# Performance work log

Hardware: AMD Instinct MI355X
Metric: run time of the kernel (lower is better)

## Reference

```python
import jax, jax.numpy as jnp
import numpy as np

B, CIN, H, W = 8, 512, 32, 32
NH = 8
DQ = DK = DV = 256  # int(0.5 * Cin)
COUT = 512


def setup_inputs() -> dict:
    key = jax.random.key(0)
    k0, k1, k2, k3, k4 = jax.random.split(key, 5)
    x = jax.random.normal(k0, (B, CIN, H, W), dtype=jnp.float32)
    # 1x1 conv weights stored as [out, in] matrices (kernel size 1)
    w_qkv = jax.random.normal(k1, (DQ + DK + DV, CIN), dtype=jnp.float32) * 0.02
    b_qkv = jax.random.normal(k2, (DQ + DK + DV,), dtype=jnp.float32) * 0.02
    w_attn = jax.random.normal(k3, (COUT, DV), dtype=jnp.float32) * 0.02
    b_attn = jax.random.normal(k4, (COUT,), dtype=jnp.float32) * 0.02
    return {"x": x, "w_qkv": w_qkv, "b_qkv": b_qkv, "w_attn": w_attn, "b_attn": b_attn}


def _split_heads(t):
    b, c, h, w = t.shape
    return t.reshape(b, NH, c // NH, h, w)


def reference(x, w_qkv, b_qkv, w_attn, b_attn):
    b, _, h, w = x.shape
    hw = h * w
    # 1x1 conv == per-pixel GEMM
    qkv = jnp.einsum('bchw,oc->bohw', x, w_qkv) + b_qkv[None, :, None, None]
    q = qkv[:, :DQ]
    k = qkv[:, DQ:DQ + DK]
    v = qkv[:, DQ + DK:]
    dkh = DK // NH
    q = _split_heads(q) * (dkh ** -0.5)
    k = _split_heads(k)
    v = _split_heads(v)
    flat_q = q.reshape(b, NH, DQ // NH, hw)
    flat_k = k.reshape(b, NH, DK // NH, hw)
    flat_v = v.reshape(b, NH, DV // NH, hw)
    # logits: [b, NH, hw, hw]  (q^T k over feature dim)
    logits = jnp.einsum('bndq,bndk->bnqk', flat_q, flat_k)
    # FAITHFUL quirk: softmax over the HEAD axis (dim=1), as in the source
    weights = jax.nn.softmax(logits, axis=1)
    # attn_out: [b, NH, hw, dvh]
    attn_out = jnp.einsum('bnqk,bndk->bnqd', weights, flat_v)
    # FAITHFUL quirk: raw reshape (no transpose) to [b, NH, dvh, H, W]
    attn_out = attn_out.reshape(b, NH, DV // NH, h, w).reshape(b, DV, h, w)
    out = jnp.einsum('bchw,oc->bohw', attn_out, w_attn) + b_attn[None, :, None, None]
    return out
```

## Files before the change

kernel.cpp:

```cpp
#include <hip/hip_runtime.h>
#include <math.h>

#define BATCH 8
#define CIN   512
#define DQKV  768
#define NHEAD 8
#define HW    1024

typedef __attribute__((ext_vector_type(8))) short  short8;
typedef __attribute__((ext_vector_type(4))) float  float4v;

__device__ __forceinline__ ushort f2bf(float f) {
    union { float f; unsigned u; } c; c.f = f;
    unsigned u = c.u + 0x7fffu + ((c.u >> 16) & 1u);
    return (ushort)(u >> 16);
}

__device__ __forceinline__ void async_ld16(const ushort* g, ushort* l) {
    auto gp = (const __attribute__((address_space(1))) unsigned int*)g;
    auto lp = (__attribute__((address_space(3))) unsigned int*)l;
    __builtin_amdgcn_global_load_lds(gp, lp, 16, 0, 0);
}

__global__ __launch_bounds__(256)
void transpose_cvt(const float* __restrict__ in, ushort* __restrict__ out,
                   int K, int N)
{
    __shared__ float Ts[64][65];
    const int b  = blockIdx.z;
    const int k0 = blockIdx.y * 64;
    const int n0 = blockIdx.x * 64;
    const int t  = threadIdx.x;
    const float* ib = in + (size_t)b * K * N;
    ushort*      ob = out + (size_t)b * N * K;

    const int r  = t >> 4;
    const int c4 = (t & 15) * 4;
    #pragma unroll
    for (int p = 0; p < 4; ++p) {
        float4 v = *(const float4*)(ib + (size_t)(k0 + r + 16 * p) * N + n0 + c4);
        Ts[r + 16 * p][c4 + 0] = v.x;
        Ts[r + 16 * p][c4 + 1] = v.y;
        Ts[r + 16 * p][c4 + 2] = v.z;
        Ts[r + 16 * p][c4 + 3] = v.w;
    }
    __syncthreads();

    const int nl = t >> 3;
    const int kc = (t & 7) * 8;
    #pragma unroll
    for (int p = 0; p < 2; ++p) {
        int n = nl + 32 * p;
        uint4 u;
        u.x = (uint)f2bf(Ts[kc + 0][n]) | ((uint)f2bf(Ts[kc + 1][n]) << 16);
        u.y = (uint)f2bf(Ts[kc + 2][n]) | ((uint)f2bf(Ts[kc + 3][n]) << 16);
        u.z = (uint)f2bf(Ts[kc + 4][n]) | ((uint)f2bf(Ts[kc + 5][n]) << 16);
        u.w = (uint)f2bf(Ts[kc + 6][n]) | ((uint)f2bf(Ts[kc + 7][n]) << 16);
        *(uint4*)(ob + (size_t)(n0 + n) * K + k0 + kc) = u;
    }
}

__global__ void cvt_bf16(const float* __restrict__ in, ushort* __restrict__ out, int n8)
{
    int i = blockIdx.x * blockDim.x + threadIdx.x;
    if (i >= n8) return;
    const float4* p = (const float4*)(in + (size_t)i * 8);
    float4 a = p[0], b = p[1];
    uint4 u;
    u.x = (uint)f2bf(a.x) | ((uint)f2bf(a.y) << 16);
    u.y = (uint)f2bf(a.z) | ((uint)f2bf(a.w) << 16);
    u.z = (uint)f2bf(b.x) | ((uint)f2bf(b.y) << 16);
    u.w = (uint)f2bf(b.z) | ((uint)f2bf(b.w) << 16);
    *(uint4*)(out + (size_t)i * 8) = u;
}

__global__ __launch_bounds__(256)
void qk_transform(const ushort* __restrict__ qkv, ushort* __restrict__ Qt,
                  ushort* __restrict__ Kt)
{
    __shared__ ushort Ts[32 * 264];
    const int b   = blockIdx.z;
    const int g   = blockIdx.y;
    const int sp0 = blockIdx.x * 256;
    const int t   = threadIdx.x;

    const ushort* src = qkv + ((size_t)b * DQKV + g * 32) * HW;
    ushort* dst = (g < 8 ? Qt : Kt) + ((size_t)b * NHEAD + (g & 7)) * (HW * 32);

    #pragma unroll
    for (int p = 0; p < 4; ++p) {
        int d = (t >> 5) + p * 8;
        int c = t & 31;
        uint4 u = *(const uint4*)(src + (size_t)d * HW + sp0 + c * 8);
        *(uint4*)&Ts[d * 264 + c * 8] = u;
    }
    __syncthreads();

    ushort* orow = dst + (size_t)(sp0 + t) * 32;
    #pragma unroll
    for (int c = 0; c < 4; ++c) {
        ushort v[8];
        #pragma unroll
        for (int j = 0; j < 8; ++j) v[j] = Ts[(c * 8 + j) * 264 + t];
        *(uint4*)(orow + c * 8) = *(uint4*)v;
    }
}

template<int M, int K, bool QSCALE, bool OUTBF>
__global__ __launch_bounds__(256, 2)
void gemm_bt(const ushort* __restrict__ A, const ushort* __restrict__ Bt,
             const float* __restrict__ bias, void* __restrict__ Oo)
{
    __shared__ __align__(16) ushort As[128 * 64];
    __shared__ __align__(16) ushort Bs[128 * 64];

    const int b    = blockIdx.z;
    const int m0   = blockIdx.y * 128;
    const int n0   = blockIdx.x * 128;
    const int t    = threadIdx.x;
    const int lane = t & 63;
    const int wave = t >> 6;
    const int l16  = lane & 15;
    const int quad = lane >> 4;
    const int wm   = (wave & 1) * 64;
    const int wn   = (wave >> 1) * 64;

    const ushort* Bb = Bt + (size_t)b * HW * K;

    float4v acc[4][4];
    #pragma unroll
    for (int i = 0; i < 4; ++i)
        #pragma unroll
        for (int j = 0; j < 4; ++j)
            acc[i][j] = (float4v){0.f, 0.f, 0.f, 0.f};

    const int srow = t >> 3;
    const int sg   = t & 7;

    for (int k0 = 0; k0 < K; k0 += 64) {
        __syncthreads();
        #pragma unroll
        for (int is = 0; is < 4; ++is) {
            int row = srow + is * 32;
            int gch = sg ^ (row & 7);
            async_ld16(A  + (size_t)(m0 + row) * K + k0 + gch * 8,
                       As + (size_t)t * 8 + is * 2048);
            async_ld16(Bb + (size_t)(n0 + row) * K + k0 + gch * 8,
                       Bs + (size_t)t * 8 + is * 2048);
        }
        __syncthreads();

        #pragma unroll
        for (int ks = 0; ks < 2; ++ks) {
            short8 af[4], bf[4];
            #pragma unroll
            for (int i = 0; i < 4; ++i) {
                int row = wm + i * 16 + l16;
                int ch  = (ks * 4 + quad) ^ (row & 7);
                af[i] = *(const short8*)&As[row * 64 + ch * 8];
            }
            #pragma unroll
            for (int j = 0; j < 4; ++j) {
                int row = wn + j * 16 + l16;
                int ch  = (ks * 4 + quad) ^ (row & 7);
                bf[j] = *(const short8*)&Bs[row * 64 + ch * 8];
            }
            #pragma unroll
            for (int i = 0; i < 4; ++i)
                #pragma unroll
                for (int j = 0; j < 4; ++j)
                    acc[i][j] = __builtin_amdgcn_mfma_f32_16x16x32_bf16(
                        af[i], bf[j], acc[i][j], 0, 0, 0);
        }
    }

    #pragma unroll
    for (int i = 0; i < 4; ++i) {
        #pragma unroll
        for (int rr = 0; rr < 4; ++rr) {
            int m = m0 + wm + i * 16 + quad * 4 + rr;
            float bi = bias[m];
            float sc = QSCALE ? ((m < 256) ? 0.17677669529663687f : 1.0f) : 1.0f;
            #pragma unroll
            for (int j = 0; j < 4; ++j) {
                int n = n0 + wn + j * 16 + l16;
                float val = (acc[i][j][rr] + bi) * sc;
                if (OUTBF)
                    ((ushort*)Oo)[((size_t)b * M + m) * HW + n] = f2bf(val);
                else
                    ((float*)Oo)[((size_t)b * M + m) * HW + n] = val;
            }
        }
    }
}

#define WROW 136

__global__ __launch_bounds__(512, 2)
void attn_kernel(const ushort* __restrict__ qkv, const ushort* __restrict__ Qt,
                 const ushort* __restrict__ Kt, ushort* __restrict__ ab)
{
    __shared__ __align__(16) ushort Ws[NHEAD * 32 * WROW];

    const int t    = threadIdx.x;
    const int b    = blockIdx.y;
    const int q0   = blockIdx.x * 32;
    const int wave = t >> 6;
    const int lane = t & 63;
    const int l16  = lane & 15;
    const int quad = lane >> 4;

    const ushort* Vb  = qkv + ((size_t)b * DQKV + 512) * HW;
    const ushort* Qtb = Qt + (size_t)b * (NHEAD * HW * 32);
    const ushort* Ktb = Kt + (size_t)b * (NHEAD * HW * 32);

    short8 qf[NHEAD][2];
    #pragma unroll
    for (int h = 0; h < NHEAD; ++h)
        #pragma unroll
        for (int qs = 0; qs < 2; ++qs)
            qf[h][qs] = *(const short8*)(Qtb + ((size_t)h * HW + q0 + qs * 16 + l16) * 32 + quad * 8);

    float4v oacc[2][2];
    #pragma unroll
    for (int i = 0; i < 2; ++i)
        #pragma unroll
        for (int j = 0; j < 2; ++j)
            oacc[i][j] = (float4v){0.f, 0.f, 0.f, 0.f};

    for (int k0 = 0; k0 < HW; k0 += 128) {
        const int kk = k0 + wave * 16 + l16;
        float4v S[2][NHEAD];
        #pragma unroll
        for (int h = 0; h < NHEAD; ++h) {
            short8 kf = *(const short8*)(Ktb + ((size_t)h * HW + kk) * 32 + quad * 8);
            S[0][h] = __builtin_amdgcn_mfma_f32_16x16x32_bf16(
                kf, qf[h][0], (float4v){0.f, 0.f, 0.f, 0.f}, 0, 0, 0);
            S[1][h] = __builtin_amdgcn_mfma_f32_16x16x32_bf16(
                kf, qf[h][1], (float4v){0.f, 0.f, 0.f, 0.f}, 0, 0, 0);
        }

        uint2 wpk[2][NHEAD];
        #pragma unroll
        for (int qs = 0; qs < 2; ++qs) {
            float4v mx = S[qs][0];
            #pragma unroll
            for (int h = 1; h < NHEAD; ++h)
                #pragma unroll
                for (int r = 0; r < 4; ++r) mx[r] = fmaxf(mx[r], S[qs][h][r]);
            float e[NHEAD][4];
            float4v sum = (float4v){0.f, 0.f, 0.f, 0.f};
            #pragma unroll
            for (int h = 0; h < NHEAD; ++h)
                #pragma unroll
                for (int r = 0; r < 4; ++r) {
                    e[h][r] = __expf(S[qs][h][r] - mx[r]);
                    sum[r] += e[h][r];
                }
            float4v inv;
            #pragma unroll
            for (int r = 0; r < 4; ++r) inv[r] = __builtin_amdgcn_rcpf(sum[r]);
            #pragma unroll
            for (int h = 0; h < NHEAD; ++h) {
                uint2 pk;
                pk.x = (uint)f2bf(e[h][0] * inv[0]) | ((uint)f2bf(e[h][1] * inv[1]) << 16);
                pk.y = (uint)f2bf(e[h][2] * inv[2]) | ((uint)f2bf(e[h][3] * inv[3]) << 16);
                wpk[qs][h] = pk;
            }
        }

        __syncthreads();

        #pragma unroll
        for (int qs = 0; qs < 2; ++qs)
            #pragma unroll
            for (int h = 0; h < NHEAD; ++h)
                *(uint2*)&Ws[(size_t)(h * 32 + qs * 16 + l16) * WROW + wave * 16 + quad * 4]
                    = wpk[qs][h];

        __syncthreads();

        #pragma unroll
        for (int ks = 0; ks < 4; ++ks) {
            short8 wf[2], vf[2];
            #pragma unroll
            for (int qs = 0; qs < 2; ++qs)
                wf[qs] = *(const short8*)&Ws[(size_t)(wave * 32 + qs * 16 + l16) * WROW + ks * 32 + quad * 8];
            #pragma unroll
            for (int ds = 0; ds < 2; ++ds)
                vf[ds] = *(const short8*)(Vb + (size_t)(wave * 32 + ds * 16 + l16) * HW + k0 + ks * 32 + quad * 8);
            #pragma unroll
            for (int qs = 0; qs < 2; ++qs)
                #pragma unroll
                for (int ds = 0; ds < 2; ++ds)
                    oacc[qs][ds] = __builtin_amdgcn_mfma_f32_16x16x32_bf16(
                        wf[qs], vf[ds], oacc[qs][ds], 0, 0, 0);
        }
    }

    #pragma unroll
    for (int qs = 0; qs < 2; ++qs)
        #pragma unroll
        for (int ds = 0; ds < 2; ++ds) {
            int d = ds * 16 + l16;
            #pragma unroll
            for (int r = 0; r < 4; ++r) {
                int qg = q0 + qs * 16 + quad * 4 + r;
                size_t addr = ((size_t)b * HW + (size_t)((qg & 31) * 32 + d)) * 256
                            + wave * 32 + (qg >> 5);
                ab[addr] = f2bf(oacc[qs][ds][r]);
            }
        }
}

extern "C" void kernel_launch(void* const* d_in, const int* in_sizes, int n_in,
                              void* d_out, int out_size, void* d_ws, size_t ws_size,
                              hipStream_t stream)
{
    const float* x      = (const float*)d_in[0];
    const float* w_qkv  = (const float*)d_in[1];
    const float* b_qkv  = (const float*)d_in[2];
    const float* w_attn = (const float*)d_in[3];
    const float* b_attn = (const float*)d_in[4];
    float* out = (float*)d_out;

    ushort* qkv_b = (ushort*)d_ws;
    ushort* xb    = qkv_b + 6291456;
    ushort* Qt    = xb;
    ushort* Kt    = xb + 2097152;
    ushort* ab    = xb + 4194304;
    ushort* wb1   = ab + 2097152;
    ushort* wb2   = wb1 + 393216;

    cvt_bf16<<<192, 256, 0, stream>>>(w_qkv, wb1, 49152);
    cvt_bf16<<<64, 256, 0, stream>>>(w_attn, wb2, 16384);
    transpose_cvt<<<dim3(16, 8, BATCH), 256, 0, stream>>>(x, xb, CIN, HW);

    gemm_bt<DQKV, CIN, true, true>
        <<<dim3(8, 6, BATCH), 256, 0, stream>>>(wb1, xb, b_qkv, qkv_b);

    qk_transform<<<dim3(4, 16, BATCH), 256, 0, stream>>>(qkv_b, Qt, Kt);

    attn_kernel<<<dim3(HW / 32, BATCH), 512, 0, stream>>>(qkv_b, Qt, Kt, ab);

    gemm_bt<512, 256, false, false>
        <<<dim3(8, 4, BATCH), 256, 0, stream>>>(wb2, ab, b_attn, out);
}
```

Baseline: 162.9 us.

## Halve attention query tile, remap queries for coalesced output via LDS staging

The attention kernel now handles 16 queries per block instead of 32, doubling the grid to 64x8 blocks. Each block takes a strided query set (j + 32*(uh*16+l16)), so its outputs land in contiguous columns of the raw-reshaped buffer. Results are staged through shared memory and written as 16-byte vector stores instead of scattered 2-byte stores. Halving per-thread state and raising launch bounds to 4 blocks per CU aims at higher occupancy, at the cost of reloading K and V tiles twice as often overall.

```diff
diff --git a/kernel.cpp b/kernel.cpp
--- a/kernel.cpp
+++ b/kernel.cpp
@@ -195,16 +195,18 @@
 }
 
 #define WROW 136
-
-__global__ __launch_bounds__(512, 2)
+#define OROW 132
+
+__global__ __launch_bounds__(512, 4)
 void attn_kernel(const ushort* __restrict__ qkv, const ushort* __restrict__ Qt,
                  const ushort* __restrict__ Kt, ushort* __restrict__ ab)
 {
-    __shared__ __align__(16) ushort Ws[NHEAD * 32 * WROW];
+    __shared__ __align__(16) ushort Ws[NHEAD * 16 * WROW];
 
     const int t    = threadIdx.x;
     const int b    = blockIdx.y;
-    const int q0   = blockIdx.x * 32;
+    const int j    = blockIdx.x >> 1;
+    const int uh   = blockIdx.x & 1;
     const int wave = t >> 6;
     const int lane = t & 63;
     const int l16  = lane & 15;
@@ -214,103 +216,90 @@
     const ushort* Qtb = Qt + (size_t)b * (NHEAD * HW * 32);
     const ushort* Ktb = Kt + (size_t)b * (NHEAD * HW * 32);
 
-    short8 qf[NHEAD][2];
+    const int qlane = (uh * 16 + l16) * 32 + j;
+    short8 qf[NHEAD];
     #pragma unroll
     for (int h = 0; h < NHEAD; ++h)
-        #pragma unroll
-        for (int qs = 0; qs < 2; ++qs)
-            qf[h][qs] = *(const short8*)(Qtb + ((size_t)h * HW + q0 + qs * 16 + l16) * 32 + quad * 8);
-
-    float4v oacc[2][2];
-    #pragma unroll
-    for (int i = 0; i < 2; ++i)
-        #pragma unroll
-        for (int j = 0; j < 2; ++j)
-            oacc[i][j] = (float4v){0.f, 0.f, 0.f, 0.f};
+        qf[h] = *(const short8*)(Qtb + ((size_t)h * HW + qlane) * 32 + quad * 8);
+
+    float4v oacc[2];
+    oacc[0] = (float4v){0.f, 0.f, 0.f, 0.f};
+    oacc[1] = (float4v){0.f, 0.f, 0.f, 0.f};
 
     for (int k0 = 0; k0 < HW; k0 += 128) {
         const int kk = k0 + wave * 16 + l16;
-        float4v S[2][NHEAD];
+        float4v S[NHEAD];
         #pragma unroll
         for (int h = 0; h < NHEAD; ++h) {
             short8 kf = *(const short8*)(Ktb + ((size_t)h * HW + kk) * 32 + quad * 8);
-            S[0][h] = __builtin_amdgcn_mfma_f32_16x16x32_bf16(
-                kf, qf[h][0], (float4v){0.f, 0.f, 0.f, 0.f}, 0, 0, 0);
-            S[1][h] = __builtin_amdgcn_mfma_f32_16x16x32_bf16(
-                kf, qf[h][1], (float4v){0.f, 0.f, 0.f, 0.f}, 0, 0, 0);
-        }
-
-        uint2 wpk[2][NHEAD];
-        #pragma unroll
-        for (int qs = 0; qs < 2; ++qs) {
-            float4v mx = S[qs][0];
-            #pragma unroll
-            for (int h = 1; h < NHEAD; ++h)
-                #pragma unroll
-                for (int r = 0; r < 4; ++r) mx[r] = fmaxf(mx[r], S[qs][h][r]);
-            float e[NHEAD][4];
-            float4v sum = (float4v){0.f, 0.f, 0.f, 0.f};
-            #pragma unroll
-            for (int h = 0; h < NHEAD; ++h)
-                #pragma unroll
-                for (int r = 0; r < 4; ++r) {
-                    e[h][r] = __expf(S[qs][h][r] - mx[r]);
-                    sum[r] += e[h][r];
-                }
-            float4v inv;
-            #pragma unroll
-            for (int r = 0; r < 4; ++r) inv[r] = __builtin_amdgcn_rcpf(sum[r]);
-            #pragma unroll
-            for (int h = 0; h < NHEAD; ++h) {
-                uint2 pk;
-                pk.x = (uint)f2bf(e[h][0] * inv[0]) | ((uint)f2bf(e[h][1] * inv[1]) << 16);
-                pk.y = (uint)f2bf(e[h][2] * inv[2]) | ((uint)f2bf(e[h][3] * inv[3]) << 16);
-                wpk[qs][h] = pk;
-            }
+            S[h] = __builtin_amdgcn_mfma_f32_16x16x32_bf16(
+                kf, qf[h], (float4v){0.f, 0.f, 0.f, 0.f}, 0, 0, 0);
+        }
+
+        float4v mx = S[0];
+        #pragma unroll
+        for (int h = 1; h < NHEAD; ++h)
+            #pragma unroll
+            for (int r = 0; r < 4; ++r) mx[r] = fmaxf(mx[r], S[h][r]);
+        float4v sum = (float4v){0.f, 0.f, 0.f, 0.f};
+        #pragma unroll
+        for (int h = 0; h < NHEAD; ++h)
+            #pragma unroll
+            for (int r = 0; r < 4; ++r) {
+                S[h][r] = __expf(S[h][r] - mx[r]);
+                sum[r] += S[h][r];
+            }
+        float4v inv;
+        #pragma unroll
+        for (int r = 0; r < 4; ++r) inv[r] = __builtin_amdgcn_rcpf(sum[r]);
+        uint2 wpk[NHEAD];
+        #pragma unroll
+        for (int h = 0; h < NHEAD; ++h) {
+            wpk[h].x = (uint)f2bf(S[h][0] * inv[0]) | ((uint)f2bf(S[h][1] * inv[1]) << 16);
+            wpk[h].y = (uint)f2bf(S[h][2] * inv[2]) | ((uint)f2bf(S[h][3] * inv[3]) << 16);
         }
 
         __syncthreads();
 
         #pragma unroll
-        for (int qs = 0; qs < 2; ++qs)
-            #pragma unroll
-            for (int h = 0; h < NHEAD; ++h)
-                *(uint2*)&Ws[(size_t)(h * 32 + qs * 16 + l16) * WROW + wave * 16 + quad * 4]
-                    = wpk[qs][h];
+        for (int h = 0; h < NHEAD; ++h)
+            *(uint2*)&Ws[(size_t)(h * 16 + l16) * WROW + wave * 16 + quad * 4] = wpk[h];
 
         __syncthreads();
 
         #pragma unroll
         for (int ks = 0; ks < 4; ++ks) {
-            short8 wf[2], vf[2];
-            #pragma unroll
-            for (int qs = 0; qs < 2; ++qs)
-                wf[qs] = *(const short8*)&Ws[(size_t)(wave * 32 + qs * 16 + l16) * WROW + ks * 32 + quad * 8];
-            #pragma unroll
-            for (int ds = 0; ds < 2; ++ds)
-                vf[ds] = *(const short8*)(Vb + (size_t)(wave * 32 + ds * 16 + l16) * HW + k0 + ks * 32 + quad * 8);
-            #pragma unroll
-            for (int qs = 0; qs < 2; ++qs)
-                #pragma unroll
-                for (int ds = 0; ds < 2; ++ds)
-                    oacc[qs][ds] = __builtin_amdgcn_mfma_f32_16x16x32_bf16(
-                        wf[qs], vf[ds], oacc[qs][ds], 0, 0, 0);
-        }
-    }
-
-    #pragma unroll
-    for (int qs = 0; qs < 2; ++qs)
-        #pragma unroll
-        for (int ds = 0; ds < 2; ++ds) {
-            int d = ds * 16 + l16;
-            #pragma unroll
-            for (int r = 0; r < 4; ++r) {
-                int qg = q0 + qs * 16 + quad * 4 + r;
-                size_t addr = ((size_t)b * HW + (size_t)((qg & 31) * 32 + d)) * 256
-                            + wave * 32 + (qg >> 5);
-                ab[addr] = f2bf(oacc[qs][ds][r]);
-            }
-        }
+            short8 wf = *(const short8*)&Ws[(size_t)(wave * 16 + l16) * WROW + ks * 32 + quad * 8];
+            #pragma unroll
+            for (int ds = 0; ds < 2; ++ds) {
+                short8 vf = *(const short8*)(Vb + (size_t)(wave * 32 + ds * 16 + l16) * HW
+                                             + k0 + ks * 32 + quad * 8);
+                oacc[ds] = __builtin_amdgcn_mfma_f32_16x16x32_bf16(wf, vf, oacc[ds], 0, 0, 0);
+            }
+        }
+    }
+
+    __syncthreads();
+    ushort* Ot = Ws;
+    #pragma unroll
+    for (int ds = 0; ds < 2; ++ds) {
+        int d = ds * 16 + l16;
+        #pragma unroll
+        for (int r = 0; r < 4; ++r)
+            Ot[(size_t)d * OROW + wave * 16 + quad * 4 + r] = f2bf(oacc[ds][r]);
+    }
+    __syncthreads();
+
+    {
+        int d  = t >> 4;
+        int c8 = (t & 15) * 8;
+        uint2 a = *(const uint2*)&Ot[(size_t)d * OROW + c8];
+        uint2 b2 = *(const uint2*)&Ot[(size_t)d * OROW + c8 + 4];
+        int h   = c8 >> 4;
+        int col = h * 32 + uh * 16 + (c8 & 15);
+        uint4 u = make_uint4(a.x, a.y, b2.x, b2.y);
+        *(uint4*)(ab + ((size_t)b * HW + j * 32 + d) * 256 + col) = u;
+    }
 }
 
 extern "C" void kernel_launch(void* const* d_in, const int* in_sizes, int n_in,
@@ -341,7 +330,7 @@
 
     qk_transform<<<dim3(4, 16, BATCH), 256, 0, stream>>>(qkv_b, Qt, Kt);
 
-    attn_kernel<<<dim3(HW / 32, BATCH), 512, 0, stream>>>(qkv_b, Qt, Kt, ab);
+    attn_kernel<<<dim3(64, BATCH), 512, 0, stream>>>(qkv_b, Qt, Kt, ab);
 
     gemm_bt<512, 256, false, false>
         <<<dim3(8, 4, BATCH), 256, 0, stream>>>(wb2, ab, b_attn, out);
```

After: 164.1 us. Within noise of the previous version (+0.7%).
